# Optimization experiments

Hardware: AMD Instinct MI355X
Metric: run time of the kernel (lower is better)

## Reference

```python
import jax, jax.numpy as jnp
import numpy as np

_EPS = 1e-6

def _qmul(q1, q2):  # xyzw quaternion product
    x1, y1, z1, w1 = q1[..., 0], q1[..., 1], q1[..., 2], q1[..., 3]
    x2, y2, z2, w2 = q2[..., 0], q2[..., 1], q2[..., 2], q2[..., 3]
    return jnp.stack([
        w1 * x2 + x1 * w2 + y1 * z2 - z1 * y2,
        w1 * y2 + y1 * w2 + z1 * x2 - x1 * z2,
        w1 * z2 + z1 * w2 + x1 * y2 - y1 * x2,
        w1 * w2 - x1 * x2 - y1 * y2 - z1 * z2], axis=-1)

def _qrot(q, v):  # rotate v by unit quaternion q (xyzw)
    qv, qw = q[..., :3], q[..., 3:4]
    t = 2.0 * jnp.cross(qv, v)
    return v + qw * t + jnp.cross(qv, t)

def _so3_log(q):  # quaternion (xyzw) -> rotation vector phi
    qv, qw = q[..., :3], q[..., 3:4]
    n2 = jnp.sum(qv * qv, axis=-1, keepdims=True)
    small = n2 < _EPS * _EPS
    n = jnp.sqrt(jnp.where(small, 1.0, n2))
    factor = jnp.where(small,
                       2.0 / qw - (2.0 / 3.0) * n2 / qw ** 3,
                       2.0 * jnp.arctan2(n, qw) / n)
    return factor * qv

def _so3_exp(phi):  # rotation vector -> quaternion (xyzw)
    t2 = jnp.sum(phi * phi, axis=-1, keepdims=True)
    small = t2 < _EPS * _EPS
    theta = jnp.sqrt(jnp.where(small, 1.0, t2))
    half = 0.5 * theta
    s = jnp.where(small, 0.5 - t2 / 48.0, jnp.sin(half) / theta)
    w = jnp.where(small, 1.0 - t2 / 8.0, jnp.cos(half))
    return jnp.concatenate([s * phi, w], axis=-1)

def _jl(phi, v):  # SO3 left Jacobian J_l(phi) @ v
    t2 = jnp.sum(phi * phi, axis=-1, keepdims=True)
    small = t2 < _EPS * _EPS
    t2s = jnp.where(small, 1.0, t2)
    theta = jnp.sqrt(t2s)
    a = jnp.where(small, 0.5 - t2 / 24.0, (1.0 - jnp.cos(theta)) / t2s)
    b = jnp.where(small, 1.0 / 6.0 - t2 / 120.0, (theta - jnp.sin(theta)) / (t2s * theta))
    c1 = jnp.cross(phi, v)
    return v + a * c1 + b * jnp.cross(phi, c1)

def _jl_inv(phi, v):  # SO3 left Jacobian inverse J_l^{-1}(phi) @ v
    t2 = jnp.sum(phi * phi, axis=-1, keepdims=True)
    small = t2 < _EPS * _EPS
    t2s = jnp.where(small, 1.0, t2)
    theta = jnp.sqrt(t2s)
    s = jnp.sin(theta)
    s_safe = jnp.where(jnp.abs(s) < _EPS, _EPS, s)
    c = jnp.where(small, 1.0 / 12.0 + t2 / 720.0,
                  1.0 / t2s - (1.0 + jnp.cos(theta)) / (2.0 * theta * s_safe))
    c1 = jnp.cross(phi, v)
    return v - 0.5 * c1 + c * jnp.cross(phi, c1)

def _se3_inv(T):
    t, q = T[..., :3], T[..., 3:]
    qi = q * jnp.array([-1.0, -1.0, -1.0, 1.0], dtype=T.dtype)
    return jnp.concatenate([-_qrot(qi, t), qi], axis=-1)

def _se3_mul(T1, T2):
    t1, q1 = T1[..., :3], T1[..., 3:]
    t2, q2 = T2[..., :3], T2[..., 3:]
    return jnp.concatenate([t1 + _qrot(q1, t2), _qmul(q1, q2)], axis=-1)

def _se3_log(T):  # SE3 -> se3 [tau, phi]
    t, q = T[..., :3], T[..., 3:]
    phi = _so3_log(q)
    return jnp.concatenate([_jl_inv(phi, t), phi], axis=-1)

def _se3_exp(xi):  # se3 [tau, phi] -> SE3
    tau, phi = xi[..., :3], xi[..., 3:]
    q = _so3_exp(phi)
    return jnp.concatenate([_jl(phi, tau), q], axis=-1)

def _forward(input_poses, time):
    # duplicate first/last pose (inter_begin_and_end=True)
    poses = jnp.concatenate([input_poses[:, :1], input_poses, input_poses[:, -1:]], axis=1)
    B, P = poses.shape[0], poses.shape[1]
    S = P - 3  # number of spline segments
    u = time.reshape(-1)  # [K]
    K = u.shape[0]
    U = jnp.stack([jnp.ones_like(u), u, u * u, u * u * u], axis=0)  # [4,K]
    M = jnp.array([[5., 3., -3., 1.], [1., 3., 3., -2.], [0., 0., 0., 1.]], dtype=u.dtype) / 6.0
    w = M @ U  # [3,K] cumulative B-spline weights
    p0, p1 = poses[:, 0:S], poses[:, 1:S + 1]
    p2, p3 = poses[:, 2:S + 2], poses[:, 3:S + 3]
    d0 = _se3_log(_se3_mul(_se3_inv(p0), p1))  # [B,S,6]
    d1 = _se3_log(_se3_mul(_se3_inv(p1), p2))
    d2 = _se3_log(_se3_mul(_se3_inv(p2), p3))
    A0 = _se3_exp(d0[:, :, None, :] * w[0][None, None, :, None])  # [B,S,K,7]
    A1 = _se3_exp(d1[:, :, None, :] * w[1][None, None, :, None])
    A2 = _se3_exp(d2[:, :, None, :] * w[2][None, None, :, None])
    Td = jnp.broadcast_to(p0[:, :, None, :], (B, S, K, 7))
    out = _se3_mul(_se3_mul(_se3_mul(Td, A0), A1), A2)
    return out.reshape(B, S * K, 7)

def setup_inputs() -> dict:
    key = jax.random.key(0)
    k1, k2, k3 = jax.random.split(key, 3)
    B, N, K = 32, 2048, 32
    t = jax.random.normal(k1, (B, N, 3), dtype=jnp.float32) * 2.0
    q = jax.random.normal(k2, (B, N, 4), dtype=jnp.float32)
    q = q / jnp.linalg.norm(q, axis=-1, keepdims=True)
    q = jnp.where(q[..., 3:4] < 0, -q, q)  # qw >= 0 for well-conditioned Log
    input_poses = jnp.concatenate([t, q], axis=-1)
    time = jax.random.uniform(k3, (1, 1, K), dtype=jnp.float32)
    return {"input_poses": input_poses, "time": time}

def reference(input_poses, time):
    return _forward(input_poses, time)
```

## Files before the change

kernel.cpp:

```cpp
#include <hip/hip_runtime.h>
#include <cmath>

namespace {

typedef _Float16 half_t;
typedef _Float16 h2 __attribute__((ext_vector_type(2)));

constexpr int BATCH  = 32;
constexpr int NPOSE  = 2048;
constexpr int KSAMP  = 32;
constexpr int NSEG   = NPOSE - 1;
constexpr int NDELTA = NPOSE + 1;
constexpr int SEGB   = 32;
constexpr float EPS  = 1e-6f;
constexpr float EPS2 = 1e-12f;
constexpr float INV_TWO_PI = 0.15915494309189535f;

struct V3 { float x, y, z; };
struct Q4 { float x, y, z, w; };
struct SE3 { V3 t; Q4 q; };

__device__ __forceinline__ float frcp(float x)  { return __builtin_amdgcn_rcpf(x); }
__device__ __forceinline__ float fsqrt(float x) { return __builtin_amdgcn_sqrtf(x); }
__device__ __forceinline__ float fsin(float x)  { return __builtin_amdgcn_sinf(x * INV_TWO_PI); }
__device__ __forceinline__ float fcos(float x)  { return __builtin_amdgcn_cosf(x * INV_TWO_PI); }

__device__ __forceinline__ h2 h2pack(float a, float b) { return h2{(half_t)a, (half_t)b}; }
__device__ __forceinline__ h2 h2splat(float a) { half_t h = (half_t)a; return h2{h, h}; }

__device__ __forceinline__ V3 v3add(V3 a, V3 b) { return {a.x + b.x, a.y + b.y, a.z + b.z}; }
__device__ __forceinline__ V3 v3sub(V3 a, V3 b) { return {a.x - b.x, a.y - b.y, a.z - b.z}; }
__device__ __forceinline__ V3 v3scl(V3 a, float s) { return {a.x * s, a.y * s, a.z * s}; }
__device__ __forceinline__ float v3dot(V3 a, V3 b) { return a.x * b.x + a.y * b.y + a.z * b.z; }
__device__ __forceinline__ V3 v3cross(V3 a, V3 b) {
    return {a.y * b.z - a.z * b.y, a.z * b.x - a.x * b.z, a.x * b.y - a.y * b.x};
}

__device__ __forceinline__ V3 qrot(Q4 q, V3 v) {
    V3 qv{q.x, q.y, q.z};
    V3 t = v3scl(v3cross(qv, v), 2.0f);
    return v3add(v3add(v, v3scl(t, q.w)), v3cross(qv, t));
}

__device__ __forceinline__ Q4 qmul(Q4 a, Q4 b) {
    return {a.w * b.x + a.x * b.w + a.y * b.z - a.z * b.y,
            a.w * b.y + a.y * b.w + a.z * b.x - a.x * b.z,
            a.w * b.z + a.z * b.w + a.x * b.y - a.y * b.x,
            a.w * b.w - a.x * b.x - a.y * b.y - a.z * b.z};
}

__device__ __forceinline__ float facos(float x) {
    float ax = fabsf(x);
    float p = -0.0012624911f;
    p = p * ax + 0.0066700901f;
    p = p * ax - 0.0170881256f;
    p = p * ax + 0.0308918810f;
    p = p * ax - 0.0501743046f;
    p = p * ax + 0.0889789874f;
    p = p * ax - 0.2145988016f;
    p = p * ax + 1.5707963050f;
    float r = fsqrt(fmaxf(1.0f - ax, 0.0f)) * p;
    return (x >= 0.0f) ? r : (3.14159265358979f - r);
}

__device__ __forceinline__ V3 so3_log(Q4 q) {
    V3 qv{q.x, q.y, q.z};
    float n2 = v3dot(qv, qv);
    bool small = n2 < EPS2;
    float n = fsqrt(small ? 1.0f : n2);
    float iw = frcp(q.w);
    float f_small = 2.0f * iw - (2.0f / 3.0f) * n2 * iw * iw * iw;
    float wc = fminf(fmaxf(q.w, -1.0f), 1.0f);
    float f_big = 2.0f * facos(wc) * frcp(n);
    return v3scl(qv, small ? f_small : f_big);
}

__device__ __forceinline__ V3 jl_inv(V3 phi, V3 v) {
    float t2 = v3dot(phi, phi);
    bool small = t2 < EPS2;
    float t2s = small ? 1.0f : t2;
    float theta = fsqrt(t2s);
    float s = fsin(theta), cth = fcos(theta);
    float s_safe = (fabsf(s) < EPS) ? EPS : s;
    float c_big = frcp(t2s) - (1.0f + cth) * frcp(2.0f * theta * s_safe);
    float c = small ? (1.0f / 12.0f + t2 * (1.0f / 720.0f)) : c_big;
    V3 c1 = v3cross(phi, v);
    return v3add(v3sub(v, v3scl(c1, 0.5f)), v3scl(v3cross(phi, c1), c));
}

struct V3h { h2 x, y, z; };
struct Q4h { h2 x, y, z, w; };
struct SE3h { V3h t; Q4h q; };

__device__ __forceinline__ SE3h se3_mul_h(const SE3h& A, const SE3h& B) {
    h2 cx = A.q.y * B.t.z - A.q.z * B.t.y;
    h2 cy = A.q.z * B.t.x - A.q.x * B.t.z;
    h2 cz = A.q.x * B.t.y - A.q.y * B.t.x;
    cx = cx + cx; cy = cy + cy; cz = cz + cz;
    SE3h r;
    r.t.x = A.t.x + B.t.x + A.q.w * cx + (A.q.y * cz - A.q.z * cy);
    r.t.y = A.t.y + B.t.y + A.q.w * cy + (A.q.z * cx - A.q.x * cz);
    r.t.z = A.t.z + B.t.z + A.q.w * cz + (A.q.x * cy - A.q.y * cx);
    r.q.x = A.q.w * B.q.x + A.q.x * B.q.w + A.q.y * B.q.z - A.q.z * B.q.y;
    r.q.y = A.q.w * B.q.y + A.q.y * B.q.w + A.q.z * B.q.x - A.q.x * B.q.z;
    r.q.z = A.q.w * B.q.z + A.q.z * B.q.w + A.q.x * B.q.y - A.q.y * B.q.x;
    r.q.w = A.q.w * B.q.w - A.q.x * B.q.x - A.q.y * B.q.y - A.q.z * B.q.z;
    return r;
}

__device__ __forceinline__ SE3h build_E(const float4& A, const float4& U,
                                        const float4& C1, const float4& C2,
                                        float wa, float wb) {
    const float inv_n = U.w;
    float tha = wa * A.w, thb = wb * A.w;
    float sa = fsin(0.5f * tha), ca = fcos(0.5f * tha);
    float sb = fsin(0.5f * thb), cb = fcos(0.5f * thb);
    float cAa = 2.0f * sa * sa * inv_n;
    float cAb = 2.0f * sb * sb * inv_n;
    float cBa = (tha - 2.0f * sa * ca) * inv_n;
    float cBb = (thb - 2.0f * sb * cb) * inv_n;
    h2 s2 = h2pack(sa, sb), c2 = h2pack(ca, cb);
    h2 cA = h2pack(cAa, cAb), cB = h2pack(cBa, cBb), wh = h2pack(wa, wb);
    SE3h E;
    E.q.x = s2 * h2splat(U.x); E.q.y = s2 * h2splat(U.y); E.q.z = s2 * h2splat(U.z);
    E.q.w = c2;
    E.t.x = wh * h2splat(A.x) + cA * h2splat(C1.x) + cB * h2splat(C2.x);
    E.t.y = wh * h2splat(A.y) + cA * h2splat(C1.y) + cB * h2splat(C2.y);
    E.t.z = wh * h2splat(A.z) + cA * h2splat(C1.z) + cB * h2splat(C2.z);
    return E;
}

__global__ __launch_bounds__(256) void lie_spline_fused(
    const float* __restrict__ poses,
    const float* __restrict__ timev,
    float* __restrict__ out)
{
    __shared__ float4 sdel[(SEGB + 2) * 5];
    __shared__ __align__(16) float stage[SEGB * KSAMP * 7];

    const int b   = blockIdx.y;
    const int s0  = blockIdx.x * SEGB;
    const int tid = threadIdx.x;

    const int segl = tid >> 3;
    const int m    = tid & 7;
    const int s    = s0 + segl;

    int ip = min(max(s - 1, 0), NPOSE - 1);
    const float* P0 = poses + ((size_t)b * NPOSE + ip) * 7;
    const float4 uvec = reinterpret_cast<const float4*>(timev)[m];
    SE3h Tph;
    Tph.t.x = h2splat(P0[0]); Tph.t.y = h2splat(P0[1]); Tph.t.z = h2splat(P0[2]);
    Tph.q.x = h2splat(P0[3]); Tph.q.y = h2splat(P0[4]); Tph.q.z = h2splat(P0[5]);
    Tph.q.w = h2splat(P0[6]);

    if (tid < SEGB + 2) {
        int i = min(s0 + tid, NDELTA - 1);
        int ia = max(i - 1, 0);
        int ib = min(i, NPOSE - 1);
        const float* Pa = poses + ((size_t)b * NPOSE + ia) * 7;
        const float* Pb = poses + ((size_t)b * NPOSE + ib) * 7;
        V3 ta{Pa[0], Pa[1], Pa[2]}; Q4 qa{Pa[3], Pa[4], Pa[5], Pa[6]};
        V3 tb{Pb[0], Pb[1], Pb[2]}; Q4 qb{Pb[3], Pb[4], Pb[5], Pb[6]};

        Q4 qi{-qa.x, -qa.y, -qa.z, qa.w};
        V3 trel = qrot(qi, v3sub(tb, ta));
        Q4 qrel = qmul(qi, qb);
        V3 phi = so3_log(qrel);
        V3 tau = jl_inv(phi, trel);

        float nphi = fsqrt(v3dot(phi, phi));
        float inv_n = frcp(fmaxf(nphi, 1e-20f));
        V3 u  = v3scl(phi, inv_n);
        V3 c1 = v3cross(u, tau);
        V3 c2 = v3cross(u, c1);

        float4* r = sdel + tid * 5;
        r[0] = make_float4(tau.x, tau.y, tau.z, nphi);
        r[1] = make_float4(u.x,  u.y,  u.z,  inv_n);
        r[2] = make_float4(c1.x, c1.y, c1.z, 0.0f);
        r[3] = make_float4(c2.x, c2.y, c2.z, 0.0f);
    }
    __syncthreads();

    if (s < NSEG) {
        const float4* R = sdel + segl * 5;
        const float4 A0 = R[0],  U0 = R[1],  C10 = R[2],  C20 = R[3];
        const float4 A1 = R[5],  U1 = R[6],  C11 = R[7],  C21 = R[8];
        const float4 A2 = R[10], U2 = R[11], C12 = R[12], C22 = R[13];

        const float c6 = 1.0f / 6.0f;
        SE3h TA, TB;
        #define POSE_PAIR(ua_, ub_, Tdst_)                                       \
        {                                                                        \
            float ua = (ua_), ub = (ub_);                                        \
            float ua2 = ua * ua, ua3 = ua2 * ua;                                 \
            float ub2 = ub * ub, ub3 = ub2 * ub;                                 \
            float w0a = (5.0f + 3.0f * ua - 3.0f * ua2 + ua3) * c6;              \
            float w0b = (5.0f + 3.0f * ub - 3.0f * ub2 + ub3) * c6;              \
            float w1a = (1.0f + 3.0f * ua + 3.0f * ua2 - 2.0f * ua3) * c6;       \
            float w1b = (1.0f + 3.0f * ub + 3.0f * ub2 - 2.0f * ub3) * c6;       \
            float w2a = ua3 * c6, w2b = ub3 * c6;                                \
            SE3h T = se3_mul_h(Tph, build_E(A0, U0, C10, C20, w0a, w0b));        \
            T = se3_mul_h(T, build_E(A1, U1, C11, C21, w1a, w1b));               \
            T = se3_mul_h(T, build_E(A2, U2, C12, C22, w2a, w2b));               \
            Tdst_ = T;                                                           \
        }
        POSE_PAIR(uvec.x, uvec.y, TA)
        POSE_PAIR(uvec.z, uvec.w, TB)
        #undef POSE_PAIR

        float4* sv = reinterpret_cast<float4*>(stage + segl * (KSAMP * 7) + m * 28);
        sv[0] = make_float4((float)TA.t.x.x, (float)TA.t.y.x, (float)TA.t.z.x, (float)TA.q.x.x);
        sv[1] = make_float4((float)TA.q.y.x, (float)TA.q.z.x, (float)TA.q.w.x, (float)TA.t.x.y);
        sv[2] = make_float4((float)TA.t.y.y, (float)TA.t.z.y, (float)TA.q.x.y, (float)TA.q.y.y);
        sv[3] = make_float4((float)TA.q.z.y, (float)TA.q.w.y, (float)TB.t.x.x, (float)TB.t.y.x);
        sv[4] = make_float4((float)TB.t.z.x, (float)TB.q.x.x, (float)TB.q.y.x, (float)TB.q.z.x);
        sv[5] = make_float4((float)TB.q.w.x, (float)TB.t.x.y, (float)TB.t.y.y, (float)TB.t.z.y);
        sv[6] = make_float4((float)TB.q.x.y, (float)TB.q.y.y, (float)TB.q.z.y, (float)TB.q.w.y);
    }
    __syncthreads();

    int nseg_blk = min(NSEG - s0, SEGB);
    int nvec = nseg_blk * (KSAMP * 7 / 4);
    const float4* svv = reinterpret_cast<const float4*>(stage);
    float4* ov = reinterpret_cast<float4*>(out + ((size_t)b * NSEG + s0) * (size_t)(KSAMP * 7));
    for (int j = tid; j < nvec; j += 256) ov[j] = svv[j];
}

}

extern "C" void kernel_launch(void* const* d_in, const int* in_sizes, int n_in,
                              void* d_out, int out_size, void* d_ws, size_t ws_size,
                              hipStream_t stream) {
    const float* poses = (const float*)d_in[0];
    const float* timev = (const float*)d_in[1];
    float* out = (float*)d_out;
    (void)in_sizes; (void)n_in; (void)out_size; (void)d_ws; (void)ws_size;

    dim3 grid((NSEG + SEGB - 1) / SEGB, BATCH);
    lie_spline_fused<<<grid, 256, 0, stream>>>(poses, timev, out);
}
```

Before: 80.42 us.

## Switch pose chain to packed fp32, store outputs directly, share poses via LDS

Replaces the packed fp16 pose composition with packed fp32 (float2 vectors), which removes the half conversions and raises precision. Each thread now writes its two samples straight to global memory instead of staging a 28 KB LDS tile and copying it out after a second barrier. The base pose is read from the shared delta record rather than by a per-thread global load. The per-thread direct stores are less coalesced than the block-wide copy, and fp32 math doubles the ALU width relative to packed fp16, in exchange for lower LDS use, higher occupancy and one fewer barrier.

After: 86.99 us. 1.08x slower.

```diff
diff --git a/kernel.cpp b/kernel.cpp
--- a/kernel.cpp
+++ b/kernel.cpp
@@ -3,8 +3,7 @@
 
 namespace {
 
-typedef _Float16 half_t;
-typedef _Float16 h2 __attribute__((ext_vector_type(2)));
+typedef float f2 __attribute__((ext_vector_type(2)));
 
 constexpr int BATCH  = 32;
 constexpr int NPOSE  = 2048;
@@ -12,21 +11,18 @@
 constexpr int NSEG   = NPOSE - 1;
 constexpr int NDELTA = NPOSE + 1;
 constexpr int SEGB   = 32;
+constexpr int RSTRIDE = 7;
 constexpr float EPS  = 1e-6f;
 constexpr float EPS2 = 1e-12f;
 constexpr float INV_TWO_PI = 0.15915494309189535f;
 
 struct V3 { float x, y, z; };
 struct Q4 { float x, y, z, w; };
-struct SE3 { V3 t; Q4 q; };
 
 __device__ __forceinline__ float frcp(float x)  { return __builtin_amdgcn_rcpf(x); }
 __device__ __forceinline__ float fsqrt(float x) { return __builtin_amdgcn_sqrtf(x); }
 __device__ __forceinline__ float fsin(float x)  { return __builtin_amdgcn_sinf(x * INV_TWO_PI); }
 __device__ __forceinline__ float fcos(float x)  { return __builtin_amdgcn_cosf(x * INV_TWO_PI); }
-
-__device__ __forceinline__ h2 h2pack(float a, float b) { return h2{(half_t)a, (half_t)b}; }
-__device__ __forceinline__ h2 h2splat(float a) { half_t h = (half_t)a; return h2{h, h}; }
 
 __device__ __forceinline__ V3 v3add(V3 a, V3 b) { return {a.x + b.x, a.y + b.y, a.z + b.z}; }
 __device__ __forceinline__ V3 v3sub(V3 a, V3 b) { return {a.x - b.x, a.y - b.y, a.z - b.z}; }
@@ -88,16 +84,18 @@
     return v3add(v3sub(v, v3scl(c1, 0.5f)), v3scl(v3cross(phi, c1), c));
 }
 
-struct V3h { h2 x, y, z; };
-struct Q4h { h2 x, y, z, w; };
-struct SE3h { V3h t; Q4h q; };
-
-__device__ __forceinline__ SE3h se3_mul_h(const SE3h& A, const SE3h& B) {
-    h2 cx = A.q.y * B.t.z - A.q.z * B.t.y;
-    h2 cy = A.q.z * B.t.x - A.q.x * B.t.z;
-    h2 cz = A.q.x * B.t.y - A.q.y * B.t.x;
+struct V3p { f2 x, y, z; };
+struct Q4p { f2 x, y, z, w; };
+struct SE3p { V3p t; Q4p q; };
+
+__device__ __forceinline__ f2 splat(float a) { return f2{a, a}; }
+
+__device__ __forceinline__ SE3p se3_mul_p(const SE3p& A, const SE3p& B) {
+    f2 cx = A.q.y * B.t.z - A.q.z * B.t.y;
+    f2 cy = A.q.z * B.t.x - A.q.x * B.t.z;
+    f2 cz = A.q.x * B.t.y - A.q.y * B.t.x;
     cx = cx + cx; cy = cy + cy; cz = cz + cz;
-    SE3h r;
+    SE3p r;
     r.t.x = A.t.x + B.t.x + A.q.w * cx + (A.q.y * cz - A.q.z * cy);
     r.t.y = A.t.y + B.t.y + A.q.w * cy + (A.q.z * cx - A.q.x * cz);
     r.t.z = A.t.z + B.t.z + A.q.w * cz + (A.q.x * cy - A.q.y * cx);
@@ -108,7 +106,7 @@
     return r;
 }
 
-__device__ __forceinline__ SE3h build_E(const float4& A, const float4& U,
+__device__ __forceinline__ SE3p build_E(const float4& A, const float4& U,
                                         const float4& C1, const float4& C2,
                                         float wa, float wb) {
     const float inv_n = U.w;
@@ -119,14 +117,14 @@
     float cAb = 2.0f * sb * sb * inv_n;
     float cBa = (tha - 2.0f * sa * ca) * inv_n;
     float cBb = (thb - 2.0f * sb * cb) * inv_n;
-    h2 s2 = h2pack(sa, sb), c2 = h2pack(ca, cb);
-    h2 cA = h2pack(cAa, cAb), cB = h2pack(cBa, cBb), wh = h2pack(wa, wb);
-    SE3h E;
-    E.q.x = s2 * h2splat(U.x); E.q.y = s2 * h2splat(U.y); E.q.z = s2 * h2splat(U.z);
+    f2 s2{sa, sb}, c2{ca, cb};
+    f2 cA{cAa, cAb}, cB{cBa, cBb}, wh{wa, wb};
+    SE3p E;
+    E.q.x = s2 * splat(U.x); E.q.y = s2 * splat(U.y); E.q.z = s2 * splat(U.z);
     E.q.w = c2;
-    E.t.x = wh * h2splat(A.x) + cA * h2splat(C1.x) + cB * h2splat(C2.x);
-    E.t.y = wh * h2splat(A.y) + cA * h2splat(C1.y) + cB * h2splat(C2.y);
-    E.t.z = wh * h2splat(A.z) + cA * h2splat(C1.z) + cB * h2splat(C2.z);
+    E.t.x = wh * splat(A.x) + cA * splat(C1.x) + cB * splat(C2.x);
+    E.t.y = wh * splat(A.y) + cA * splat(C1.y) + cB * splat(C2.y);
+    E.t.z = wh * splat(A.z) + cA * splat(C1.z) + cB * splat(C2.z);
     return E;
 }
 
@@ -135,8 +133,7 @@
     const float* __restrict__ timev,
     float* __restrict__ out)
 {
-    __shared__ float4 sdel[(SEGB + 2) * 5];
-    __shared__ __align__(16) float stage[SEGB * KSAMP * 7];
+    __shared__ float4 sdel[(SEGB + 2) * RSTRIDE];
 
     const int b   = blockIdx.y;
     const int s0  = blockIdx.x * SEGB;
@@ -145,14 +142,6 @@
     const int segl = tid >> 3;
     const int m    = tid & 7;
     const int s    = s0 + segl;
-
-    int ip = min(max(s - 1, 0), NPOSE - 1);
-    const float* P0 = poses + ((size_t)b * NPOSE + ip) * 7;
-    const float4 uvec = reinterpret_cast<const float4*>(timev)[m];
-    SE3h Tph;
-    Tph.t.x = h2splat(P0[0]); Tph.t.y = h2splat(P0[1]); Tph.t.z = h2splat(P0[2]);
-    Tph.q.x = h2splat(P0[3]); Tph.q.y = h2splat(P0[4]); Tph.q.z = h2splat(P0[5]);
-    Tph.q.w = h2splat(P0[6]);
 
     if (tid < SEGB + 2) {
         int i = min(s0 + tid, NDELTA - 1);
@@ -175,23 +164,36 @@
         V3 c1 = v3cross(u, tau);
         V3 c2 = v3cross(u, c1);
 
-        float4* r = sdel + tid * 5;
+        float4* r = sdel + tid * RSTRIDE;
         r[0] = make_float4(tau.x, tau.y, tau.z, nphi);
         r[1] = make_float4(u.x,  u.y,  u.z,  inv_n);
         r[2] = make_float4(c1.x, c1.y, c1.z, 0.0f);
         r[3] = make_float4(c2.x, c2.y, c2.z, 0.0f);
+        r[4] = make_float4(ta.x, ta.y, ta.z, qa.x);
+        r[5] = make_float4(qa.y, qa.z, qa.w, 0.0f);
     }
     __syncthreads();
 
     if (s < NSEG) {
-        const float4* R = sdel + segl * 5;
-        const float4 A0 = R[0],  U0 = R[1],  C10 = R[2],  C20 = R[3];
-        const float4 A1 = R[5],  U1 = R[6],  C11 = R[7],  C21 = R[8];
-        const float4 A2 = R[10], U2 = R[11], C12 = R[12], C22 = R[13];
+        const float4* R = sdel + segl * RSTRIDE;
+        const float4 A0 = R[0],             U0 = R[1],             C10 = R[2],             C20 = R[3];
+        const float4 P03 = R[4],            P46 = R[5];
+        const float4 A1 = R[RSTRIDE],       U1 = R[RSTRIDE + 1],   C11 = R[RSTRIDE + 2],   C21 = R[RSTRIDE + 3];
+        const float4 A2 = R[2 * RSTRIDE],   U2 = R[2 * RSTRIDE + 1], C12 = R[2 * RSTRIDE + 2], C22 = R[2 * RSTRIDE + 3];
+
+        const float4 uvec = reinterpret_cast<const float4*>(timev)[m];
+
+        SE3p Tph;
+        Tph.t.x = splat(P03.x); Tph.t.y = splat(P03.y); Tph.t.z = splat(P03.z);
+        Tph.q.x = splat(P03.w); Tph.q.y = splat(P46.x); Tph.q.z = splat(P46.y);
+        Tph.q.w = splat(P46.z);
+
+        float* obase = out + ((size_t)b * NSEG + s) * (size_t)(KSAMP * 7) + m * 28;
+        float4* o4 = reinterpret_cast<float4*>(obase);
+        float2* o2 = reinterpret_cast<float2*>(obase);
 
         const float c6 = 1.0f / 6.0f;
-        SE3h TA, TB;
-        #define POSE_PAIR(ua_, ub_, Tdst_)                                       \
+        #define CHAIN(ua_, ub_, Tdst_)                                           \
         {                                                                        \
             float ua = (ua_), ub = (ub_);                                        \
             float ua2 = ua * ua, ua3 = ua2 * ua;                                 \
@@ -201,31 +203,30 @@
             float w1a = (1.0f + 3.0f * ua + 3.0f * ua2 - 2.0f * ua3) * c6;       \
             float w1b = (1.0f + 3.0f * ub + 3.0f * ub2 - 2.0f * ub3) * c6;       \
             float w2a = ua3 * c6, w2b = ub3 * c6;                                \
-            SE3h T = se3_mul_h(Tph, build_E(A0, U0, C10, C20, w0a, w0b));        \
-            T = se3_mul_h(T, build_E(A1, U1, C11, C21, w1a, w1b));               \
-            T = se3_mul_h(T, build_E(A2, U2, C12, C22, w2a, w2b));               \
+            SE3p T = se3_mul_p(Tph, build_E(A0, U0, C10, C20, w0a, w0b));        \
+            T = se3_mul_p(T, build_E(A1, U1, C11, C21, w1a, w1b));               \
+            T = se3_mul_p(T, build_E(A2, U2, C12, C22, w2a, w2b));               \
             Tdst_ = T;                                                           \
         }
-        POSE_PAIR(uvec.x, uvec.y, TA)
-        POSE_PAIR(uvec.z, uvec.w, TB)
-        #undef POSE_PAIR
-
-        float4* sv = reinterpret_cast<float4*>(stage + segl * (KSAMP * 7) + m * 28);
-        sv[0] = make_float4((float)TA.t.x.x, (float)TA.t.y.x, (float)TA.t.z.x, (float)TA.q.x.x);
-        sv[1] = make_float4((float)TA.q.y.x, (float)TA.q.z.x, (float)TA.q.w.x, (float)TA.t.x.y);
-        sv[2] = make_float4((float)TA.t.y.y, (float)TA.t.z.y, (float)TA.q.x.y, (float)TA.q.y.y);
-        sv[3] = make_float4((float)TA.q.z.y, (float)TA.q.w.y, (float)TB.t.x.x, (float)TB.t.y.x);
-        sv[4] = make_float4((float)TB.t.z.x, (float)TB.q.x.x, (float)TB.q.y.x, (float)TB.q.z.x);
-        sv[5] = make_float4((float)TB.q.w.x, (float)TB.t.x.y, (float)TB.t.y.y, (float)TB.t.z.y);
-        sv[6] = make_float4((float)TB.q.x.y, (float)TB.q.y.y, (float)TB.q.z.y, (float)TB.q.w.y);
+
+        {
+            SE3p TA;
+            CHAIN(uvec.x, uvec.y, TA)
+            o4[0] = make_float4(TA.t.x[0], TA.t.y[0], TA.t.z[0], TA.q.x[0]);
+            o4[1] = make_float4(TA.q.y[0], TA.q.z[0], TA.q.w[0], TA.t.x[1]);
+            o4[2] = make_float4(TA.t.y[1], TA.t.z[1], TA.q.x[1], TA.q.y[1]);
+            o2[6] = make_float2(TA.q.z[1], TA.q.w[1]);
+        }
+        {
+            SE3p TB;
+            CHAIN(uvec.z, uvec.w, TB)
+            o2[7] = make_float2(TB.t.x[0], TB.t.y[0]);
+            o4[4] = make_float4(TB.t.z[0], TB.q.x[0], TB.q.y[0], TB.q.z[0]);
+            o4[5] = make_float4(TB.q.w[0], TB.t.x[1], TB.t.y[1], TB.t.z[1]);
+            o4[6] = make_float4(TB.q.x[1], TB.q.y[1], TB.q.z[1], TB.q.w[1]);
+        }
+        #undef CHAIN
     }
-    __syncthreads();
-
-    int nseg_blk = min(NSEG - s0, SEGB);
-    int nvec = nseg_blk * (KSAMP * 7 / 4);
-    const float4* svv = reinterpret_cast<const float4*>(stage);
-    float4* ov = reinterpret_cast<float4*>(out + ((size_t)b * NSEG + s0) * (size_t)(KSAMP * 7));
-    for (int j = tid; j < nvec; j += 256) ov[j] = svv[j];
 }
 
 }
```
